# Kernel optimization log

Hardware: AMD Instinct MI355X
Metric: run time of the kernel (lower is better)

## Reference

```python
import jax, jax.numpy as jnp
import numpy as np

B, T, D, H = 64, 512, 1024, 1024


def setup_inputs() -> dict:
    key = jax.random.key(0)
    k1, k2, k3 = jax.random.split(key, 3)
    scale_x = 1.0 / np.sqrt(D)
    scale_h = 1.0 / np.sqrt(H)
    return {
        "x": jax.random.normal(k1, (B, T, D), dtype=jnp.float32),
        "Wx": jax.random.normal(k2, (D, H), dtype=jnp.float32) * scale_x,
        "Wh": jax.random.normal(k3, (H, H), dtype=jnp.float32) * scale_h,
        "b": jnp.zeros((H,), dtype=jnp.float32),
    }


def reference(x, Wx, Wh, b):
    # Simple RNN: h_t = tanh(x_t @ Wx + h_{t-1} @ Wh + b), h_0 = 0.
    # Precompute the input projection for all timesteps in one big GEMM.
    xp = jnp.einsum("btd,dh->bth", x, Wx) + b  # [B, T, H]

    def step(h, xp_t):
        h_new = jnp.tanh(xp_t + h @ Wh)  # [B, H]
        return h_new, h_new

    h0 = jnp.zeros((x.shape[0], Wh.shape[0]), dtype=x.dtype)
    _, hs = jax.lax.scan(step, h0, jnp.swapaxes(xp, 0, 1))  # hs: [T, B, H]
    return jnp.swapaxes(hs, 0, 1)  # [B, T, H]
```

## Files before the change

kernel.cpp:

```cpp
#include <hip/hip_runtime.h>
#include <hip/hip_bf16.h>
#include <hip/hip_fp16.h>
#include <cstddef>

#define BATCH 64
#define TT    512
#define DD    1024
#define HH    1024

typedef _Float16 f16x8 __attribute__((ext_vector_type(8)));
typedef _Float16 f16x4 __attribute__((ext_vector_type(4)));
typedef float    f32x4 __attribute__((ext_vector_type(4)));
typedef unsigned long long u64;

union H8U2 { f16x8 v; u64 u[2]; };
union H4U1 { f16x4 h; u64 u; };
union F16P { _Float16 h[2]; unsigned u; };

#define MFMA16(a, b, c) __builtin_amdgcn_mfma_f32_16x16x32_f16((a), (b), (c), 0, 0, 0)

__device__ __forceinline__ float fast_tanh(float x) {
    float ax = __builtin_fabsf(x);
    float e  = __expf(-2.0f * ax);
    float r  = (1.0f - e) * __builtin_amdgcn_rcpf(1.0f + e);
    unsigned ur = (__float_as_uint(r) & 0x7fffffffu) | (__float_as_uint(x) & 0x80000000u);
    return __uint_as_float(ur);
}

__global__ __launch_bounds__(256) void convert_w(
    const float* __restrict__ W, _Float16* __restrict__ Wf,
    u64* __restrict__ hzero)
{
    if (hzero && blockIdx.x < 128)
        hzero[(size_t)blockIdx.x * 256 + threadIdx.x] = 0ull;

    int o2   = blockIdx.x * 256 + threadIdx.x;
    int idx  = o2 * 2;
    int e    = idx & 7;
    int lane = (idx >> 3) & 63;
    int G    = idx >> 9;
    int kk   = G & 31;
    int cg   = G >> 5;
    int c    = cg * 16 + (lane & 15);
    int k    = kk * 32 + ((lane >> 4) & 3) * 8 + e;

    float v0 = W[(size_t)k * 1024 + c];
    float v1 = W[(size_t)(k + 1) * 1024 + c];
    F16P p; p.h[0] = (_Float16)v0; p.h[1] = (_Float16)v1;
    ((unsigned*)Wf)[o2] = p.u;
}

__global__ __launch_bounds__(256, 1) void gemm_xp_mfma(
    const float* __restrict__ x,
    const _Float16* __restrict__ WxA,
    const float* __restrict__ bias,
    float* __restrict__ out)
{
    const int w    = threadIdx.x >> 6;
    const int lane = threadIdx.x & 63;
    const int l15  = lane & 15;
    const int lq   = lane >> 4;
    const int token0 = (blockIdx.x * 4 + w) * 16;

    f16x8 bfrag[32];
    {
        const float* xb = x + (size_t)(token0 + l15) * DD + lq * 8;
#pragma unroll
        for (int kk = 0; kk < 32; ++kk) {
            f32x4 lo = *(const f32x4*)(xb + kk * 32);
            f32x4 hi = *(const f32x4*)(xb + kk * 32 + 4);
            f16x8 f;
#pragma unroll
            for (int j = 0; j < 4; ++j) { f[j] = (_Float16)lo[j]; f[4 + j] = (_Float16)hi[j]; }
            bfrag[kk] = f;
        }
    }
#pragma unroll
    for (int kk = 0; kk < 32; ++kk) asm volatile("" : "+v"(bfrag[kk]));

    const size_t outb = (size_t)(token0 + l15) * HH + 4 * lq;

    for (int i = 0; i < 64; ++i) {
        const int cg = (i + blockIdx.x) & 63;
        const f16x8* ap = (const f16x8*)WxA + (size_t)cg * 32 * 64 + lane;
        f16x8 a[32];
#pragma unroll
        for (int kk = 0; kk < 32; ++kk) a[kk] = ap[(size_t)kk * 64];

        f32x4 acc0 = {0,0,0,0}, acc1 = {0,0,0,0}, acc2 = {0,0,0,0}, acc3 = {0,0,0,0};
#pragma unroll
        for (int q = 0; q < 8; ++q) {
            acc0 = MFMA16(a[q*4+0], bfrag[q*4+0], acc0);
            acc1 = MFMA16(a[q*4+1], bfrag[q*4+1], acc1);
            acc2 = MFMA16(a[q*4+2], bfrag[q*4+2], acc2);
            acc3 = MFMA16(a[q*4+3], bfrag[q*4+3], acc3);
        }
        f32x4 bv = *(const f32x4*)(bias + cg * 16 + 4 * lq);
        f32x4 r;
#pragma unroll
        for (int v = 0; v < 4; ++v)
            r[v] = ((acc0[v] + acc1[v]) + (acc2[v] + acc3[v])) + bv[v];
        *(f32x4*)(out + outb + cg * 16) = r;
    }
}

__global__ __launch_bounds__(256, 1) void rnn_persist(
    const _Float16* __restrict__ Whf,
    _Float16* __restrict__ hb0,
    _Float16* __restrict__ hb1,
    float* __restrict__ out)
{
    __shared__ char ldsraw[65536];

    const int tid  = threadIdx.x;
    const int bg   = blockIdx.x & 3;
    const int co4  = blockIdx.x >> 2;
    const int w    = tid >> 6;
    const int cg   = co4 * 4 + w;
    const int lane = tid & 63;
    const int l15  = lane & 15;
    const int lq   = lane >> 4;

    f16x8 afrag[32];
    {
        const f16x8* wp = (const f16x8*)Whf + (size_t)cg * 32 * 64 + lane;
#pragma unroll
        for (int kk = 0; kk < 32; ++kk) afrag[kk] = wp[(size_t)kk * 64];
    }
#pragma unroll
    for (int kk = 0; kk < 32; ++kk) asm volatile("" : "+v"(afrag[kk]));

    _Float16* hbuf[2] = {hb0, hb1};

    const int b = bg * 16 + l15;
    const int c = cg * 16 + 4 * lq;
    const size_t ob = (size_t)b * TT * HH + c;

    unsigned soff[8];
    const _Float16* src0[8];
    const _Float16* src1[8];
    unsigned ownm = 0u;
#pragma unroll
    for (int i = 0; i < 8; ++i) {
        int gi   = tid + 256 * i;
        int srow = gi >> 7;
        int scol = gi & 127;
        soff[i]  = ((unsigned)gi * 16u) ^ (unsigned)((srow & 7) << 4);
        src0[i]  = hb0 + (size_t)(bg * 16 + srow) * HH + scol * 8;
        src1[i]  = hb1 + (size_t)(bg * 16 + srow) * HH + scol * 8;
        if ((scol >> 3) == co4) ownm |= (1u << i);
    }

    const unsigned g16 = (unsigned)(c >> 3);
    const unsigned eb  = (unsigned)(l15 * 2048)
                       + ((g16 * 16u) ^ (unsigned)((l15 & 7) << 4))
                       + 8u * (unsigned)(lq & 1);

    f32x4 xq;
    {
        const float* xpp = out + ob;
        asm volatile("global_load_dwordx4 %0, %1, off" : "=v"(xq) : "v"(xpp));
    }

    H8U2 uu[8];

    for (int t = 0; t < TT; ++t) {
        if (t > 0) {
            const unsigned tagr = 1u + (unsigned)((t - 1) % 3);
            const _Float16* const* src = ((t + 1) & 1) ? src1 : src0;

            __builtin_amdgcn_sched_barrier(0);
            asm volatile("s_waitcnt vmcnt(2)" ::: "memory");
            __builtin_amdgcn_sched_barrier(0);

            while (true) {
                unsigned good = 1u;
#pragma unroll
                for (int i = 0; i < 8; ++i) {
                    u64 lo = uu[i].u[0], hi = uu[i].u[1];
                    unsigned ta = (unsigned)(lo & 1u) | (((unsigned)(lo >> 32) & 1u) << 1);
                    unsigned tb = (unsigned)(hi & 1u) | (((unsigned)(hi >> 32) & 1u) << 1);
                    unsigned ok = (unsigned)(ta == tagr) & (unsigned)(tb == tagr);
                    good &= (ok | ((ownm >> i) & 1u));
                }
                if (__all((int)good)) break;
                __builtin_amdgcn_s_sleep(1);
#pragma unroll
                for (int i = 0; i < 8; ++i)
                    asm volatile("global_load_dwordx4 %0, %1, off sc0 sc1"
                                 : "=v"(uu[i].v) : "v"(src[i]));
                __builtin_amdgcn_sched_barrier(0);
                asm volatile("s_waitcnt vmcnt(0)" ::: "memory");
                __builtin_amdgcn_sched_barrier(0);
            }

            char* lb = ldsraw + (t & 1) * 32768;
#pragma unroll
            for (int i = 0; i < 8; ++i)
                if (!((ownm >> i) & 1u))
                    *(f16x8*)(lb + soff[i]) = uu[i].v;
        }

        asm volatile("s_waitcnt lgkmcnt(0)\n\ts_barrier" ::: "memory");

        f32x4 acc0 = {0,0,0,0}, acc1 = {0,0,0,0}, acc2 = {0,0,0,0}, acc3 = {0,0,0,0};
        if (t > 0) {
            const char* lb = ldsraw + (t & 1) * 32768;
            const unsigned rbase = (unsigned)(l15 * 2048);
            const unsigned rswz  = (unsigned)((l15 & 7) << 4);
#pragma unroll
            for (int q = 0; q < 8; ++q) {
                f16x8 b0, b1, b2, b3;
                b0 = *(const f16x8*)(lb + ((rbase + ((q*16 + 0*4 + lq) * 16u)) ^ rswz));
                b1 = *(const f16x8*)(lb + ((rbase + ((q*16 + 1*4 + lq) * 16u)) ^ rswz));
                b2 = *(const f16x8*)(lb + ((rbase + ((q*16 + 2*4 + lq) * 16u)) ^ rswz));
                b3 = *(const f16x8*)(lb + ((rbase + ((q*16 + 3*4 + lq) * 16u)) ^ rswz));
                acc0 = MFMA16(afrag[q*4+0], b0, acc0);
                acc1 = MFMA16(afrag[q*4+1], b1, acc1);
                acc2 = MFMA16(afrag[q*4+2], b2, acc2);
                acc3 = MFMA16(afrag[q*4+3], b3, acc3);
            }
        }

        __builtin_amdgcn_sched_barrier(0);
        asm volatile("s_waitcnt vmcnt(0)" ::: "memory");
        __builtin_amdgcn_sched_barrier(0);

        const unsigned tagw = 1u + (unsigned)(t % 3);
        f32x4 hvv;
        H4U1 pk;
#pragma unroll
        for (int v = 0; v < 4; ++v) {
            float s = ((acc0[v] + acc1[v]) + (acc2[v] + acc3[v])) + xq[v];
            hvv[v] = fast_tanh(s);
            pk.h[v] = (_Float16)hvv[v];
        }
        pk.u = (pk.u & ~(1ull | (1ull << 32)))
             | (u64)(tagw & 1u) | ((u64)(tagw >> 1) << 32);

        if (t + 1 < TT)
            *(u64*)(ldsraw + ((t + 1) & 1) * 32768 + eb) = pk.u;

        {
            _Float16* q = hbuf[t & 1] + (size_t)b * HH + c;
            asm volatile("global_store_dwordx2 %0, %1, off sc0 sc1"
                         :: "v"(q), "v"(pk.u) : "memory");
        }
        if (t + 1 < TT) {
            const _Float16* const* src = (t & 1) ? src1 : src0;
#pragma unroll
            for (int i = 0; i < 8; ++i)
                asm volatile("global_load_dwordx4 %0, %1, off sc0 sc1"
                             : "=v"(uu[i].v) : "v"(src[i]));
        }
        {
            const float* op = out + ob + (size_t)t * HH;
            asm volatile("global_store_dwordx4 %0, %1, off"
                         :: "v"(op), "v"(hvv) : "memory");
        }
        if (t + 1 < TT) {
            const float* xpp = out + ob + (size_t)(t + 1) * HH;
            asm volatile("global_load_dwordx4 %0, %1, off" : "=v"(xq) : "v"(xpp));
        }
    }
}

extern "C" void kernel_launch(void* const* d_in, const int* in_sizes, int n_in,
                              void* d_out, int out_size, void* d_ws, size_t ws_size,
                              hipStream_t stream) {
    const float* x    = (const float*)d_in[0];
    const float* Wx   = (const float*)d_in[1];
    const float* Wh   = (const float*)d_in[2];
    const float* bias = (const float*)d_in[3];

    float* out = (float*)d_out;

    _Float16* Whf = (_Float16*)d_ws;
    _Float16* WxA = Whf + (1u << 20);
    _Float16* hb0 = WxA + (1u << 20);
    _Float16* hb1 = hb0 + BATCH * HH;

    convert_w<<<2048, 256, 0, stream>>>(Wh, Whf, (u64*)hb0);
    convert_w<<<2048, 256, 0, stream>>>(Wx, WxA, nullptr);

    gemm_xp_mfma<<<512, 256, 0, stream>>>(x, WxA, bias, out);

    rnn_persist<<<64, 256, 0, stream>>>(Whf, hb0, hb1, out);
}
```

Baseline: 1.714 ms.

## Stage Wx tiles through double-buffered LDS and issue second speculative h poll

```diff
diff --git a/kernel.cpp b/kernel.cpp
--- a/kernel.cpp
+++ b/kernel.cpp
@@ -25,6 +25,12 @@
     float r  = (1.0f - e) * __builtin_amdgcn_rcpf(1.0f + e);
     unsigned ur = (__float_as_uint(r) & 0x7fffffffu) | (__float_as_uint(x) & 0x80000000u);
     return __uint_as_float(ur);
+}
+
+__device__ __forceinline__ unsigned tagok(u64 lo, u64 hi, unsigned tagr) {
+    unsigned ta = (unsigned)(lo & 1u) | (((unsigned)(lo >> 32) & 1u) << 1);
+    unsigned tb = (unsigned)(hi & 1u) | (((unsigned)(hi >> 32) & 1u) << 1);
+    return (unsigned)(ta == tagr) & (unsigned)(tb == tagr);
 }
 
 __global__ __launch_bounds__(256) void convert_w(
@@ -56,8 +62,11 @@
     const float* __restrict__ bias,
     float* __restrict__ out)
 {
-    const int w    = threadIdx.x >> 6;
-    const int lane = threadIdx.x & 63;
+    __shared__ char lds[2][32768];
+
+    const int tid  = threadIdx.x;
+    const int w    = tid >> 6;
+    const int lane = tid & 63;
     const int l15  = lane & 15;
     const int lq   = lane >> 4;
     const int token0 = (blockIdx.x * 4 + w) * 16;
@@ -80,20 +89,40 @@
 
     const size_t outb = (size_t)(token0 + l15) * HH + 4 * lq;
 
+    {
+        const int cg0 = blockIdx.x & 63;
+        const f16x8* gp = (const f16x8*)WxA + (size_t)cg0 * 2048;
+        f16x8 st[8];
+#pragma unroll
+        for (int j = 0; j < 8; ++j) st[j] = gp[tid + 256 * j];
+#pragma unroll
+        for (int j = 0; j < 8; ++j) *(f16x8*)(lds[0] + (tid + 256 * j) * 16) = st[j];
+    }
+    __syncthreads();
+
     for (int i = 0; i < 64; ++i) {
         const int cg = (i + blockIdx.x) & 63;
-        const f16x8* ap = (const f16x8*)WxA + (size_t)cg * 32 * 64 + lane;
-        f16x8 a[32];
-#pragma unroll
-        for (int kk = 0; kk < 32; ++kk) a[kk] = ap[(size_t)kk * 64];
-
+
+        f16x8 st[8];
+        if (i + 1 < 64) {
+            const int cgn = (i + 1 + blockIdx.x) & 63;
+            const f16x8* gp = (const f16x8*)WxA + (size_t)cgn * 2048;
+#pragma unroll
+            for (int j = 0; j < 8; ++j) st[j] = gp[tid + 256 * j];
+        }
+
+        const char* lb = lds[i & 1];
         f32x4 acc0 = {0,0,0,0}, acc1 = {0,0,0,0}, acc2 = {0,0,0,0}, acc3 = {0,0,0,0};
 #pragma unroll
         for (int q = 0; q < 8; ++q) {
-            acc0 = MFMA16(a[q*4+0], bfrag[q*4+0], acc0);
-            acc1 = MFMA16(a[q*4+1], bfrag[q*4+1], acc1);
-            acc2 = MFMA16(a[q*4+2], bfrag[q*4+2], acc2);
-            acc3 = MFMA16(a[q*4+3], bfrag[q*4+3], acc3);
+            f16x8 a0 = *(const f16x8*)(lb + ((q*4 + 0) * 64 + lane) * 16);
+            f16x8 a1 = *(const f16x8*)(lb + ((q*4 + 1) * 64 + lane) * 16);
+            f16x8 a2 = *(const f16x8*)(lb + ((q*4 + 2) * 64 + lane) * 16);
+            f16x8 a3 = *(const f16x8*)(lb + ((q*4 + 3) * 64 + lane) * 16);
+            acc0 = MFMA16(a0, bfrag[q*4+0], acc0);
+            acc1 = MFMA16(a1, bfrag[q*4+1], acc1);
+            acc2 = MFMA16(a2, bfrag[q*4+2], acc2);
+            acc3 = MFMA16(a3, bfrag[q*4+3], acc3);
         }
         f32x4 bv = *(const f32x4*)(bias + cg * 16 + 4 * lq);
         f32x4 r;
@@ -101,6 +130,13 @@
         for (int v = 0; v < 4; ++v)
             r[v] = ((acc0[v] + acc1[v]) + (acc2[v] + acc3[v])) + bv[v];
         *(f32x4*)(out + outb + cg * 16) = r;
+
+        if (i + 1 < 64) {
+            char* lw = lds[(i + 1) & 1];
+#pragma unroll
+            for (int j = 0; j < 8; ++j) *(f16x8*)(lw + (tid + 256 * j) * 16) = st[j];
+        }
+        __syncthreads();
     }
 }
 
@@ -162,7 +198,7 @@
         asm volatile("global_load_dwordx4 %0, %1, off" : "=v"(xq) : "v"(xpp));
     }
 
-    H8U2 uu[8];
+    H8U2 uu[8], uu2[8];
 
     for (int t = 0; t < TT; ++t) {
         if (t > 0) {
@@ -170,18 +206,17 @@
             const _Float16* const* src = ((t + 1) & 1) ? src1 : src0;
 
             __builtin_amdgcn_sched_barrier(0);
-            asm volatile("s_waitcnt vmcnt(2)" ::: "memory");
+            asm volatile("s_waitcnt vmcnt(1)" ::: "memory");
             __builtin_amdgcn_sched_barrier(0);
 
             while (true) {
                 unsigned good = 1u;
 #pragma unroll
                 for (int i = 0; i < 8; ++i) {
-                    u64 lo = uu[i].u[0], hi = uu[i].u[1];
-                    unsigned ta = (unsigned)(lo & 1u) | (((unsigned)(lo >> 32) & 1u) << 1);
-                    unsigned tb = (unsigned)(hi & 1u) | (((unsigned)(hi >> 32) & 1u) << 1);
-                    unsigned ok = (unsigned)(ta == tagr) & (unsigned)(tb == tagr);
-                    good &= (ok | ((ownm >> i) & 1u));
+                    unsigned ok1 = tagok(uu[i].u[0],  uu[i].u[1],  tagr);
+                    unsigned ok2 = tagok(uu2[i].u[0], uu2[i].u[1], tagr);
+                    if (!ok1) uu[i] = uu2[i];
+                    good &= (ok1 | ok2 | ((ownm >> i) & 1u));
                 }
                 if (__all((int)good)) break;
                 __builtin_amdgcn_s_sleep(1);
@@ -259,6 +294,11 @@
                          :: "v"(op), "v"(hvv) : "memory");
         }
         if (t + 1 < TT) {
+            const _Float16* const* src = (t & 1) ? src1 : src0;
+#pragma unroll
+            for (int i = 0; i < 8; ++i)
+                asm volatile("global_load_dwordx4 %0, %1, off sc0 sc1"
+                             : "=v"(uu2[i].v) : "v"(src[i]));
             const float* xpp = out + ob + (size_t)(t + 1) * HH;
             asm volatile("global_load_dwordx4 %0, %1, off" : "=v"(xq) : "v"(xpp));
         }
```

After: 2.014 ms. +17.5%, slower.
